# Kernel optimization log

Measured on AMD Instinct MI355X. Metric: run time of the kernel, lower is better.

## Reference

```python
import jax, jax.numpy as jnp
import numpy as np

# SparseSAKEEnergyModel: 6-layer sparse SAKE GNN (hidden=64, heads=4, update=False)
# followed by per-graph segment_sum and a Dense(64)->silu->Dense(1) head.
N_NODES = 10000
N_EDGES = 100000
F_IN = 16           # raw node feature dim (embedded to H by embedding_in)
H = 64              # hidden_features
HEADS = 4           # SAKE default n_heads
COEF = H * HEADS    # n_coefficients = 256
DEPTH = 6
RBF = 50            # ExpNormalSmearing num_rbf
CUT = 5.0           # ExpNormalSmearing cutoff_upper (alpha = 5/(5-0) = 1)
NUM_SEGMENTS = 100


def setup_inputs() -> dict:
    key = jax.random.key(0)
    ks = jax.random.split(key, 20)

    def dn(k, *shape):
        # Dense kernel init ~ lecun-normal-ish: std = 1/sqrt(fan_in); fan_in = shape[-2]
        return jax.random.normal(k, shape, jnp.float32) * np.float32(1.0 / np.sqrt(shape[-2]))

    start = float(np.exp(-CUT))
    rbf_means = jnp.broadcast_to(jnp.linspace(start, 1.0, RBF).astype(jnp.float32)[None], (DEPTH, RBF))
    rbf_betas = jnp.full((DEPTH, RBF), float(((2.0 / RBF) * (1.0 - start)) ** -2), jnp.float32)

    z = lambda *s: jnp.zeros(s, jnp.float32)
    return dict(
        i=jax.random.normal(ks[0], (N_NODES, F_IN), jnp.float32),
        x=jax.random.normal(ks[1], (N_NODES, 3), jnp.float32),
        emb_in_w=dn(ks[2], F_IN, H), emb_in_b=z(H),
        edge_in_w=dn(ks[3], DEPTH, 2 * H, RBF), edge_in_b=z(DEPTH, RBF),
        rbf_means=rbf_means, rbf_betas=rbf_betas,
        edge_out_w1=dn(ks[4], DEPTH, 2 * H + RBF + 1, H), edge_out_b1=z(DEPTH, H),
        edge_out_w2=dn(ks[5], DEPTH, H, H), edge_out_b2=z(DEPTH, H),
        sem_w=dn(ks[6], DEPTH, H, HEADS), sem_b=z(DEPTH, HEADS),
        xmix_w=dn(ks[7], DEPTH, COEF, COEF),
        pn_w1=dn(ks[8], DEPTH, COEF, H), pn_b1=z(DEPTH, H),
        pn_w2=dn(ks[9], DEPTH, H, H), pn_b2=z(DEPTH, H),
        node_w1=dn(ks[10], DEPTH, H + COEF + H, H), node_b1=z(DEPTH, H),
        node_w2=dn(ks[11], DEPTH, H, H), node_b2=z(DEPTH, H),
        emb_out_w1=dn(ks[12], H, H), emb_out_b1=z(H),
        emb_out_w2=dn(ks[13], H, H), emb_out_b2=z(H),
        head_w1=dn(ks[14], H, H), head_b1=z(H),
        head_w2=dn(ks[15], H, 1), head_b2=z(1),
        edges=jax.random.randint(ks[16], (N_EDGES, 2), 0, N_NODES, jnp.int32),
        graph_segments=jnp.sort(jax.random.randint(ks[17], (N_NODES,), 0, NUM_SEGMENTS, jnp.int32)),
    )


def _segment_softmax(logits, seg, num_segments):
    m = jax.ops.segment_max(logits, seg, num_segments)
    e = jnp.exp(logits - m[seg])
    s = jax.ops.segment_sum(e, seg, num_segments)
    return e / s[seg]


def _forward(i, x, emb_in_w, emb_in_b, edge_in_w, edge_in_b, rbf_means, rbf_betas,
             edge_out_w1, edge_out_b1, edge_out_w2, edge_out_b2, sem_w, sem_b, xmix_w,
             pn_w1, pn_b1, pn_w2, pn_b2, node_w1, node_b1, node_w2, node_b2,
             emb_out_w1, emb_out_b1, emb_out_w2, emb_out_b2,
             head_w1, head_b1, head_w2, head_b2, edges, graph_segments):
    N = x.shape[0]
    dst, src = edges[:, 0], edges[:, 1]
    x_minus_xt = x[dst] - x[src]                               # (E,3)
    d = jnp.sqrt((x_minus_xt ** 2).sum(-1, keepdims=True) + 1e-10)  # (E,1)
    dirs = x_minus_xt / (d + 1e-5)                             # normalized edge directions
    rbf_base = jnp.exp(-d)                                     # ExpNormalSmearing, alpha=1, lower=0

    h = i @ emb_in_w + emb_in_b                                # embedding_in -> (N,H)
    for l in range(DEPTH):
        # --- edge model: ContinuousFilterConvolutionWithConcatenation ---
        hc = jnp.concatenate([h[dst], h[src]], -1)             # (E,2H)
        hm = hc @ edge_in_w[l] + edge_in_b[l]                  # (E,RBF)
        rbf = jnp.exp(-rbf_betas[l] * (rbf_base - rbf_means[l]) ** 2)
        he = jnp.concatenate([hc, rbf * hm, d], -1)
        he = jax.nn.silu(he @ edge_out_w1[l] + edge_out_b1[l]) @ edge_out_w2[l] + edge_out_b2[l]  # (E,H)
        # --- combined (semantic * euclidean) attention, segment-softmax over dst ---
        att_s = _segment_softmax(jax.nn.celu(he @ sem_w[l] + sem_b[l], alpha=2.0), dst, N)  # (E,HEADS)
        att_e = _segment_softmax(-d, dst, N)                   # (E,1)
        att = att_e * att_s
        att = att / jax.ops.segment_sum(att, dst, N)[dst]
        hea = (he[:, :, None] * att[:, None, :]).reshape(-1, COEF)  # (E, H*HEADS)
        # --- spatial attention ---
        coef = jnp.tanh(hea @ xmix_w[l])                       # (E,COEF)
        csum = jax.ops.segment_sum(coef[:, :, None] * dirs[:, None, :], dst, N)  # (N,COEF,3)
        cnorm = (csum ** 2).sum(-1)                            # (N,COEF)
        h_comb = jax.nn.silu(jax.nn.silu(cnorm @ pn_w1[l] + pn_b1[l]) @ pn_w2[l] + pn_b2[l])
        # --- aggregate + node update (residual) ---
        h_agg = jax.ops.segment_sum(hea, dst, N)               # (N,COEF)
        upd = jnp.concatenate([h, h_agg, h_comb], -1)
        upd = jax.nn.silu(jax.nn.silu(upd @ node_w1[l] + node_b1[l]) @ node_w2[l] + node_b2[l])
        h = h + upd
    h = jax.nn.silu(h @ emb_out_w1 + emb_out_b1) @ emb_out_w2 + emb_out_b2  # embedding_out
    y = jax.ops.segment_sum(h, graph_segments, NUM_SEGMENTS)   # per-graph readout (G,H)
    return jax.nn.silu(y @ head_w1 + head_b1) @ head_w2 + head_b2  # (G,1)


def reference(i, x, emb_in_w, emb_in_b, edge_in_w, edge_in_b, rbf_means, rbf_betas,
              edge_out_w1, edge_out_b1, edge_out_w2, edge_out_b2, sem_w, sem_b, xmix_w,
              pn_w1, pn_b1, pn_w2, pn_b2, node_w1, node_b1, node_w2, node_b2,
              emb_out_w1, emb_out_b1, emb_out_w2, emb_out_b2,
              head_w1, head_b1, head_w2, head_b2, edges, graph_segments):
    return _forward(i, x, emb_in_w, emb_in_b, edge_in_w, edge_in_b, rbf_means, rbf_betas,
                    edge_out_w1, edge_out_b1, edge_out_w2, edge_out_b2, sem_w, sem_b, xmix_w,
                    pn_w1, pn_b1, pn_w2, pn_b2, node_w1, node_b1, node_w2, node_b2,
                    emb_out_w1, emb_out_b1, emb_out_w2, emb_out_b2,
                    head_w1, head_b1, head_w2, head_b2, edges, graph_segments)
```

## Files before the change

### kernel.cpp

```cpp
#include <hip/hip_runtime.h>
#include <hip/hip_bf16.h>

constexpr int EN   = 100000;
constexpr int NN   = 10000;
constexpr int DEPTH = 6;
constexpr int NSEG = 100;
constexpr int LP   = 40;

typedef unsigned short u16;
typedef __bf16 bf16x8 __attribute__((ext_vector_type(8)));
typedef float  f32x4  __attribute__((ext_vector_type(4)));

__device__ inline float wred_max(float v){
#pragma unroll
  for (int o = 32; o > 0; o >>= 1) v = fmaxf(v, __shfl_xor(v, o, 64));
  return v;
}
__device__ inline float wred_sum(float v){
#pragma unroll
  for (int o = 32; o > 0; o >>= 1) v += __shfl_xor(v, o, 64);
  return v;
}
__device__ inline float siluf(float x){ return x / (1.f + __expf(-x)); }
__device__ inline float fast_tanh(float x){
  float e = __expf(2.f * x);
  return 1.f - 2.f / (e + 1.f);
}
__device__ inline u16 f2bf(float x){
  unsigned u = __float_as_uint(x);
  u = u + 0x7FFFu + ((u >> 16) & 1u);
  return (u16)(u >> 16);
}
__device__ inline float bf2f(u16 u){
  union { float f; unsigned int ui; } v; v.ui = ((unsigned int)u) << 16; return v.f;
}
__device__ inline bf16x8 ldg_bf8(const u16* p){
  return *reinterpret_cast<const bf16x8*>(p);
}

__global__ __launch_bounds__(256) void count_k(const int* __restrict__ edges,
                                               int* __restrict__ counts){
  int e = blockIdx.x * 256 + threadIdx.x;
  if (e >= EN) return;
  atomicAdd(&counts[edges[2*e]], 1);
}

__global__ __launch_bounds__(256) void scan_k(const int* __restrict__ counts,
                                              int* __restrict__ offs){
  __shared__ int part[256];
  const int CH = (NN + 255) / 256;
  int t = threadIdx.x;
  int s = 0;
  for (int j = 0; j < CH; ++j){ int idx = t*CH + j; if (idx < NN) s += counts[idx]; }
  part[t] = s;
  __syncthreads();
  if (t == 0){
    int run = 0;
    for (int i = 0; i < 256; ++i){ int v = part[i]; part[i] = run; run += v; }
    offs[NN] = run;
  }
  __syncthreads();
  int run = part[t];
  for (int j = 0; j < CH; ++j){
    int idx = t*CH + j;
    if (idx < NN){ offs[idx] = run; run += counts[idx]; }
  }
}

__global__ __launch_bounds__(256) void geoscat_k(const int* __restrict__ edges,
                                                 const float* __restrict__ x,
                                                 const int* __restrict__ offs,
                                                 int* __restrict__ cursor,
                                                 int* __restrict__ edge_s,
                                                 float* __restrict__ dS,
                                                 float* __restrict__ dirsS,
                                                 float* __restrict__ rbfS){
  int e = blockIdx.x * 256 + threadIdx.x;
  if (e >= EN) return;
  int dst = edges[2*e], src = edges[2*e+1];
  float dx = x[dst*3+0] - x[src*3+0];
  float dy = x[dst*3+1] - x[src*3+1];
  float dz = x[dst*3+2] - x[src*3+2];
  float dd = sqrtf(dx*dx + dy*dy + dz*dz + 1e-10f);
  float inv = 1.f / (dd + 1e-5f);
  int pos = offs[dst] + atomicAdd(&cursor[dst], 1);
  edge_s[2*pos]   = dst;
  edge_s[2*pos+1] = src;
  dS[pos]   = dd;
  rbfS[pos] = __expf(-dd);
  dirsS[3*pos+0] = dx*inv; dirsS[3*pos+1] = dy*inv; dirsS[3*pos+2] = dz*inv;
}

__global__ __launch_bounds__(256) void h2b_k(const float* __restrict__ h,
                                             u16* __restrict__ hbf,
                                             u16* __restrict__ node_in){
  int gid = blockIdx.x * 256 + threadIdx.x;
  if (gid >= NN*64) return;
  int n = gid >> 6, ch = gid & 63;
  u16 b = f2bf(h[gid]);
  hbf[gid] = b;
  node_in[(size_t)n*384 + ch] = b;
}

__global__ void convw_k(const float* __restrict__ src, int K, int N, size_t sStride,
                        u16* __restrict__ dst, int Kpad, int Npad, size_t dStride){
  int idx = blockIdx.x * 256 + threadIdx.x;
  if (idx >= Npad*Kpad) return;
  int n = idx / Kpad, k = idx - n*Kpad;
  float v = (k < K && n < N) ? src[blockIdx.y*sStride + (size_t)k*N + n] : 0.f;
  dst[blockIdx.y*dStride + idx] = f2bf(v);
}

__global__ __launch_bounds__(256) void convx_k(const float* __restrict__ xmix,
                                               u16* __restrict__ xr){
  int idx = blockIdx.x * 256 + threadIdx.x;
  int l = blockIdx.y;
  int q  = idx & 63;
  int n  = (idx >> 6) & 255;
  int hd = idx >> 14;
  xr[(size_t)l*65536 + idx] = f2bf(xmix[(size_t)l*65536 + (size_t)(4*q + hd)*256 + n]);
}

__global__ __launch_bounds__(256) void edge_fused_k(
    const int* __restrict__ edge_s,
    const u16* __restrict__ hbf,
    const float* __restrict__ rbfS,
    const float* __restrict__ dS,
    const u16* __restrict__ Winb,
    const float* __restrict__ bin,
    const float* __restrict__ mean,
    const float* __restrict__ beta,
    const u16* __restrict__ W1b,
    const float* __restrict__ b1,
    const u16* __restrict__ W2b,
    const float* __restrict__ b2,
    const float* __restrict__ sw,
    const float* __restrict__ sb,
    u16* __restrict__ he,
    float* __restrict__ logit){
  __shared__ u16 HC[64*132];
  __shared__ u16 T2[64*72];
  __shared__ u16 HE1[64*72];
  const int tid = threadIdx.x, lane = tid & 63, wv = tid >> 6;
  const int l15 = lane & 15, kq = (lane >> 4) * 8;
  const int rsub = (lane >> 4) << 2;
  const int e0 = blockIdx.x * 64;
  const int nw = wv*16 + l15;

#pragma unroll
  for (int i = 0; i < 4; ++i){
    int idx = tid + i*256;
    int row = idx >> 4, c = idx & 15;
    int e = min(e0 + row, EN - 1);
    int node = (c < 8) ? edge_s[2*e] : edge_s[2*e+1];
    *reinterpret_cast<uint4*>(HC + row*132 + c*8) =
        *reinterpret_cast<const uint4*>(hbf + (size_t)node*64 + (c & 7)*8);
  }
  __syncthreads();

  f32x4 acc[4];
#pragma unroll
  for (int mt = 0; mt < 4; ++mt) acc[mt] = (f32x4){0.f,0.f,0.f,0.f};
#pragma unroll
  for (int kc = 0; kc < 128; kc += 32){
    bf16x8 bf = ldg_bf8(Winb + nw*128 + kc + kq);
#pragma unroll
    for (int mt = 0; mt < 4; ++mt){
      bf16x8 af = *reinterpret_cast<const bf16x8*>(HC + (mt*16 + l15)*132 + kc + kq);
      acc[mt] = __builtin_amdgcn_mfma_f32_16x16x32_bf16(af, bf, acc[mt], 0, 0, 0);
    }
  }
  {
    float bi = 0.f, mn = 0.f, bt = 0.f;
    if (nw < 50){ bi = bin[nw]; mn = mean[nw]; bt = beta[nw]; }
#pragma unroll
    for (int mt = 0; mt < 4; ++mt){
#pragma unroll
      for (int r = 0; r < 4; ++r){
        int row = mt*16 + rsub + r;
        int e = min(e0 + row, EN - 1);
        float v;
        if (nw < 50){ float df = rbfS[e] - mn; v = __expf(-bt*df*df) * (acc[mt][r] + bi); }
        else if (nw == 50) v = dS[e];
        else v = 0.f;
        T2[row*72 + nw] = f2bf(v);
      }
    }
  }
  __syncthreads();

#pragma unroll
  for (int mt = 0; mt < 4; ++mt) acc[mt] = (f32x4){0.f,0.f,0.f,0.f};
#pragma unroll
  for (int kc = 0; kc < 128; kc += 32){
    bf16x8 bf = ldg_bf8(W1b + nw*192 + kc + kq);
#pragma unroll
    for (int mt = 0; mt < 4; ++mt){
      bf16x8 af = *reinterpret_cast<const bf16x8*>(HC + (mt*16 + l15)*132 + kc + kq);
      acc[mt] = __builtin_amdgcn_mfma_f32_16x16x32_bf16(af, bf, acc[mt], 0, 0, 0);
    }
  }
#pragma unroll
  for (int kc = 128; kc < 192; kc += 32){
    bf16x8 bf = ldg_bf8(W1b + nw*192 + kc + kq);
#pragma unroll
    for (int mt = 0; mt < 4; ++mt){
      bf16x8 af = *reinterpret_cast<const bf16x8*>(T2 + (mt*16 + l15)*72 + (kc-128) + kq);
      acc[mt] = __builtin_amdgcn_mfma_f32_16x16x32_bf16(af, bf, acc[mt], 0, 0, 0);
    }
  }
  {
    float bb = b1[nw];
#pragma unroll
    for (int mt = 0; mt < 4; ++mt){
#pragma unroll
      for (int r = 0; r < 4; ++r){
        int row = mt*16 + rsub + r;
        HE1[row*72 + nw] = f2bf(siluf(acc[mt][r] + bb));
      }
    }
  }
  __syncthreads();

#pragma unroll
  for (int mt = 0; mt < 4; ++mt) acc[mt] = (f32x4){0.f,0.f,0.f,0.f};
#pragma unroll
  for (int kc = 0; kc < 64; kc += 32){
    bf16x8 bf = ldg_bf8(W2b + nw*64 + kc + kq);
#pragma unroll
    for (int mt = 0; mt < 4; ++mt){
      bf16x8 af = *reinterpret_cast<const bf16x8*>(HE1 + (mt*16 + l15)*72 + kc + kq);
      acc[mt] = __builtin_amdgcn_mfma_f32_16x16x32_bf16(af, bf, acc[mt], 0, 0, 0);
    }
  }
  {
    float bb = b2[nw];
#pragma unroll
    for (int mt = 0; mt < 4; ++mt){
#pragma unroll
      for (int r = 0; r < 4; ++r){
        int row = mt*16 + rsub + r;
        int e = e0 + row;
        u16 hb = f2bf(acc[mt][r] + bb);
        if (e < EN) he[(size_t)e*64 + nw] = hb;
        T2[row*72 + nw] = hb;
      }
    }
  }
  __syncthreads();

  {
    int er = tid >> 2, hd = tid & 3;
    float a = sb[hd];
#pragma unroll 8
    for (int k = 0; k < 64; ++k)
      a = fmaf(bf2f(T2[er*72 + k]), sw[k*4 + hd], a);
    float v = a > 0.f ? a : 2.f*(__expf(0.5f*a) - 1.f);
    int e = e0 + er;
    if (e < EN) logit[(size_t)e*4 + hd] = v;
  }
}

__global__ __launch_bounds__(256) void xmix_k(const u16* __restrict__ he,
                                              const float* __restrict__ att,
                                              const u16* __restrict__ Xr,
                                              u16* __restrict__ coef){
  __shared__ u16 B_s[2][128*72];
  const int tid = threadIdx.x, lane = tid & 63, wave = tid >> 6;
  const int l15 = lane & 15, kq = (lane >> 4) * 8;
  const int rsub = (lane >> 4) << 2;
  const int m0 = blockIdx.x * 128;
  const int n0 = blockIdx.y * 128;

  const int srow = tid >> 1;
  const int scol = (tid & 1) * 32;
  const u16* xsrc = Xr + ((size_t)(n0 + srow))*64 + scol;

  uint4 pf0 = *reinterpret_cast<const uint4*>(xsrc);
  uint4 pf1 = *reinterpret_cast<const uint4*>(xsrc + 8);
  uint4 pf2 = *reinterpret_cast<const uint4*>(xsrc + 16);
  uint4 pf3 = *reinterpret_cast<const uint4*>(xsrc + 24);

  float a32[2][2][8];
  float4 attA[2];
#pragma unroll
  for (int h = 0; h < 2; ++h){
    int m = min(m0 + h*64 + wave*16 + l15, EN - 1);
    attA[h] = *reinterpret_cast<const float4*>(att + (size_t)m*4);
#pragma unroll
    for (int k2 = 0; k2 < 2; ++k2){
      ushort4 u0 = *reinterpret_cast<const ushort4*>(he + (size_t)m*64 + k2*32 + kq);
      ushort4 u1 = *reinterpret_cast<const ushort4*>(he + (size_t)m*64 + k2*32 + kq + 4);
      a32[h][k2][0] = bf2f(u0.x); a32[h][k2][1] = bf2f(u0.y);
      a32[h][k2][2] = bf2f(u0.z); a32[h][k2][3] = bf2f(u0.w);
      a32[h][k2][4] = bf2f(u1.x); a32[h][k2][5] = bf2f(u1.y);
      a32[h][k2][6] = bf2f(u1.z); a32[h][k2][7] = bf2f(u1.w);
    }
  }

  f32x4 acc[2][8];
#pragma unroll
  for (int h = 0; h < 2; ++h)
#pragma unroll
    for (int c = 0; c < 8; ++c) acc[h][c] = (f32x4){0.f,0.f,0.f,0.f};

  {
    u16* dst = &B_s[0][srow*72 + scol];
    *reinterpret_cast<uint4*>(dst)      = pf0;
    *reinterpret_cast<uint4*>(dst + 8)  = pf1;
    *reinterpret_cast<uint4*>(dst + 16) = pf2;
    *reinterpret_cast<uint4*>(dst + 24) = pf3;
  }
  __syncthreads();

#pragma unroll
  for (int hd = 0; hd < 4; ++hd){
    if (hd < 3){
      const u16* s = xsrc + (size_t)(hd + 1) * 256 * 64;
      pf0 = *reinterpret_cast<const uint4*>(s);
      pf1 = *reinterpret_cast<const uint4*>(s + 8);
      pf2 = *reinterpret_cast<const uint4*>(s + 16);
      pf3 = *reinterpret_cast<const uint4*>(s + 24);
    }
    bf16x8 afs[2][2];
#pragma unroll
    for (int h = 0; h < 2; ++h){
      float a = (hd==0) ? attA[h].x : (hd==1) ? attA[h].y
              : (hd==2) ? attA[h].z : attA[h].w;
#pragma unroll
      for (int k2 = 0; k2 < 2; ++k2){
        u16 o[8];
#pragma unroll
        for (int j = 0; j < 8; ++j) o[j] = f2bf(a32[h][k2][j] * a);
        afs[h][k2] = *reinterpret_cast<bf16x8*>(o);
      }
    }
    const u16* Bb = &B_s[hd & 1][0];
#pragma unroll
    for (int k2 = 0; k2 < 2; ++k2){
#pragma unroll
      for (int c = 0; c < 8; ++c){
        bf16x8 bf = *reinterpret_cast<const bf16x8*>(Bb + (c*16 + l15)*72 + k2*32 + kq);
        acc[0][c] = __builtin_amdgcn_mfma_f32_16x16x32_bf16(afs[0][k2], bf, acc[0][c], 0, 0, 0);
        acc[1][c] = __builtin_amdgcn_mfma_f32_16x16x32_bf16(afs[1][k2], bf, acc[1][c], 0, 0, 0);
      }
    }
    if (hd < 3){
      u16* dst = &B_s[(hd + 1) & 1][srow*72 + scol];
      *reinterpret_cast<uint4*>(dst)      = pf0;
      *reinterpret_cast<uint4*>(dst + 8)  = pf1;
      *reinterpret_cast<uint4*>(dst + 16) = pf2;
      *reinterpret_cast<uint4*>(dst + 24) = pf3;
      __syncthreads();
    }
  }

#pragma unroll
  for (int h = 0; h < 2; ++h){
    const int rbase = m0 + h*64 + wave*16 + rsub;
#pragma unroll
    for (int c = 0; c < 8; ++c){
      int n = n0 + c*16 + l15;
#pragma unroll
      for (int r = 0; r < 4; ++r){
        int m = rbase + r;
        if (m < EN) coef[(size_t)m*256 + n] = f2bf(acc[h][c][r]);
      }
    }
  }
}

__global__ __launch_bounds__(256) void nodeblock_k(
    const u16* __restrict__ cnorm,
    const u16* __restrict__ P1t, const float* __restrict__ pb1,
    const u16* __restrict__ P2t, const float* __restrict__ pb2,
    const u16* __restrict__ node_in,
    const u16* __restrict__ N1t, const float* __restrict__ nb1,
    const u16* __restrict__ N2t, const float* __restrict__ nb2,
    const float* __restrict__ hres,
    float* __restrict__ hout,
    u16* __restrict__ hbf,
    u16* __restrict__ node_io){
  __shared__ u16 A_s[128*LP];
  __shared__ u16 B_s[64*LP];
  __shared__ u16 T_s[128*72];
  __shared__ u16 W2_s[64*72];
  __shared__ u16 HCm[128*72];
  const int tid = threadIdx.x, lane = tid & 63, wave = tid >> 6;
  const int m0 = blockIdx.x * 128;
  const int l15 = lane & 15, kq = (lane >> 4)*8;
  const int rsub = (lane >> 4) << 2;
  const int srow = tid >> 1, skh = (tid & 1)*16;
  const int arow = min(m0 + srow, NN - 1);
  const u16* aptr1 = cnorm + (size_t)arow*256 + skh;
  const u16* aptr2 = node_in + (size_t)arow*384 + skh;
  const int brow = tid >> 2, bcol = (tid & 3)*8;

#pragma unroll
  for (int i = 0; i < 2; ++i){
    int idx = tid + i*256;
    int row = idx >> 3, cc = (idx & 7)*8;
    *reinterpret_cast<uint4*>(W2_s + row*72 + cc) =
        *reinterpret_cast<const uint4*>(P2t + row*64 + cc);
  }

  f32x4 acc0[4], acc1[4];
#pragma unroll
  for (int c = 0; c < 4; ++c){ acc0[c] = (f32x4){0,0,0,0}; acc1[c] = (f32x4){0,0,0,0}; }

  for (int kc = 0; kc < 256; kc += 32){
    *reinterpret_cast<uint4*>(A_s + srow*LP + skh)     = *reinterpret_cast<const uint4*>(aptr1 + kc);
    *reinterpret_cast<uint4*>(A_s + srow*LP + skh + 8) = *reinterpret_cast<const uint4*>(aptr1 + kc + 8);
    *reinterpret_cast<uint4*>(B_s + brow*LP + bcol) =
        *reinterpret_cast<const uint4*>(P1t + (size_t)brow*256 + kc + bcol);
    __syncthreads();
    bf16x8 af0 = *reinterpret_cast<const bf16x8*>(A_s + (wave*16 + l15)*LP + kq);
    bf16x8 af1 = *reinterpret_cast<const bf16x8*>(A_s + (64 + wave*16 + l15)*LP + kq);
#pragma unroll
    for (int c = 0; c < 4; ++c){
      bf16x8 bf = *reinterpret_cast<const bf16x8*>(B_s + (c*16 + l15)*LP + kq);
      acc0[c] = __builtin_amdgcn_mfma_f32_16x16x32_bf16(af0, bf, acc0[c], 0, 0, 0);
      acc1[c] = __builtin_amdgcn_mfma_f32_16x16x32_bf16(af1, bf, acc1[c], 0, 0, 0);
    }
    __syncthreads();
  }
#pragma unroll
  for (int h = 0; h < 2; ++h){
#pragma unroll
    for (int c = 0; c < 4; ++c){
      int n = c*16 + l15;
      float bb = pb1[n];
#pragma unroll
      for (int r = 0; r < 4; ++r){
        int rowloc = h*64 + wave*16 + rsub + r;
        float a = (h == 0) ? acc0[c][r] : acc1[c][r];
        T_s[rowloc*72 + n] = f2bf(siluf(a + bb));
      }
    }
  }
  __syncthreads();
#pragma unroll
  for (int c = 0; c < 4; ++c){ acc0[c] = (f32x4){0,0,0,0}; acc1[c] = (f32x4){0,0,0,0}; }
#pragma unroll
  for (int kc = 0; kc < 64; kc += 32){
    bf16x8 af0 = *reinterpret_cast<const bf16x8*>(T_s + (wave*16 + l15)*72 + kc + kq);
    bf16x8 af1 = *reinterpret_cast<const bf16x8*>(T_s + (64 + wave*16 + l15)*72 + kc + kq);
#pragma unroll
    for (int c = 0; c < 4; ++c){
      bf16x8 bf = *reinterpret_cast<const bf16x8*>(W2_s + (c*16 + l15)*72 + kc + kq);
      acc0[c] = __builtin_amdgcn_mfma_f32_16x16x32_bf16(af0, bf, acc0[c], 0, 0, 0);
      acc1[c] = __builtin_amdgcn_mfma_f32_16x16x32_bf16(af1, bf, acc1[c], 0, 0, 0);
    }
  }
#pragma unroll
  for (int h = 0; h < 2; ++h){
#pragma unroll
    for (int c = 0; c < 4; ++c){
      int n = c*16 + l15;
      float bb = pb2[n];
#pragma unroll
      for (int r = 0; r < 4; ++r){
        int rowloc = h*64 + wave*16 + rsub + r;
        float a = (h == 0) ? acc0[c][r] : acc1[c][r];
        HCm[rowloc*72 + n] = f2bf(siluf(a + bb));
      }
    }
  }
  __syncthreads();

#pragma unroll
  for (int c = 0; c < 4; ++c){ acc0[c] = (f32x4){0,0,0,0}; acc1[c] = (f32x4){0,0,0,0}; }
  for (int kc = 0; kc < 320; kc += 32){
    *reinterpret_cast<uint4*>(A_s + srow*LP + skh)     = *reinterpret_cast<const uint4*>(aptr2 + kc);
    *reinterpret_cast<uint4*>(A_s + srow*LP + skh + 8) = *reinterpret_cast<const uint4*>(aptr2 + kc + 8);
    *reinterpret_cast<uint4*>(B_s + brow*LP + bcol) =
        *reinterpret_cast<const uint4*>(N1t + (size_t)brow*384 + kc + bcol);
    __syncthreads();
    bf16x8 af0 = *reinterpret_cast<const bf16x8*>(A_s + (wave*16 + l15)*LP + kq);
    bf16x8 af1 = *reinterpret_cast<const bf16x8*>(A_s + (64 + wave*16 + l15)*LP + kq);
#pragma unroll
    for (int c = 0; c < 4; ++c){
      bf16x8 bf = *reinterpret_cast<const bf16x8*>(B_s + (c*16 + l15)*LP + kq);
      acc0[c] = __builtin_amdgcn_mfma_f32_16x16x32_bf16(af0, bf, acc0[c], 0, 0, 0);
      acc1[c] = __builtin_amdgcn_mfma_f32_16x16x32_bf16(af1, bf, acc1[c], 0, 0, 0);
    }
    __syncthreads();
  }
#pragma unroll
  for (int kc = 320; kc < 384; kc += 32){
    bf16x8 af0 = *reinterpret_cast<const bf16x8*>(HCm + (wave*16 + l15)*72 + (kc-320) + kq);
    bf16x8 af1 = *reinterpret_cast<const bf16x8*>(HCm + (64 + wave*16 + l15)*72 + (kc-320) + kq);
#pragma unroll
    for (int c = 0; c < 4; ++c){
      bf16x8 bf = ldg_bf8(N1t + (size_t)(c*16 + l15)*384 + kc + kq);
      acc0[c] = __builtin_amdgcn_mfma_f32_16x16x32_bf16(af0, bf, acc0[c], 0, 0, 0);
      acc1[c] = __builtin_amdgcn_mfma_f32_16x16x32_bf16(af1, bf, acc1[c], 0, 0, 0);
    }
  }
#pragma unroll
  for (int h = 0; h < 2; ++h){
#pragma unroll
    for (int c = 0; c < 4; ++c){
      int n = c*16 + l15;
      float bb = nb1[n];
#pragma unroll
      for (int r = 0; r < 4; ++r){
        int rowloc = h*64 + wave*16 + rsub + r;
        float a = (h == 0) ? acc0[c][r] : acc1[c][r];
        T_s[rowloc*72 + n] = f2bf(siluf(a + bb));
      }
    }
  }
#pragma unroll
  for (int i = 0; i < 2; ++i){
    int idx = tid + i*256;
    int row = idx >> 3, cc = (idx & 7)*8;
    *reinterpret_cast<uint4*>(W2_s + row*72 + cc) =
        *reinterpret_cast<const uint4*>(N2t + row*64 + cc);
  }
  __syncthreads();
#pragma unroll
  for (int c = 0; c < 4; ++c){ acc0[c] = (f32x4){0,0,0,0}; acc1[c] = (f32x4){0,0,0,0}; }
#pragma unroll
  for (int kc = 0; kc < 64; kc += 32){
    bf16x8 af0 = *reinterpret_cast<const bf16x8*>(T_s + (wave*16 + l15)*72 + kc + kq);
    bf16x8 af1 = *reinterpret_cast<const bf16x8*>(T_s + (64 + wave*16 + l15)*72 + kc + kq);
#pragma unroll
    for (int c = 0; c < 4; ++c){
      bf16x8 bf = *reinterpret_cast<const bf16x8*>(W2_s + (c*16 + l15)*72 + kc + kq);
      acc0[c] = __builtin_amdgcn_mfma_f32_16x16x32_bf16(af0, bf, acc0[c], 0, 0, 0);
      acc1[c] = __builtin_amdgcn_mfma_f32_16x16x32_bf16(af1, bf, acc1[c], 0, 0, 0);
    }
  }
#pragma unroll
  for (int h = 0; h < 2; ++h){
#pragma unroll
    for (int c = 0; c < 4; ++c){
      int n = c*16 + l15;
      float bb = nb2[n];
#pragma unroll
      for (int r = 0; r < 4; ++r){
        int m = m0 + h*64 + wave*16 + rsub + r;
        if (m >= NN) continue;
        float a = (h == 0) ? acc0[c][r] : acc1[c][r];
        float hn = hres[(size_t)m*64 + n] + siluf(a + bb);
        hout[(size_t)m*64 + n] = hn;
        u16 bbf = f2bf(hn);
        hbf[(size_t)m*64 + n] = bbf;
        node_io[(size_t)m*384 + n] = bbf;
      }
    }
  }
}

__global__ __launch_bounds__(256) void mlp2_head_k(const u16* __restrict__ A,
                                                   const u16* __restrict__ W1t,
                                                   const float* __restrict__ b1,
                                                   const u16* __restrict__ W2t,
                                                   const float* __restrict__ b2,
                                                   float* __restrict__ outf){
  __shared__ u16 A_s[128*LP];
  __shared__ u16 B_s[64*LP];
  __shared__ u16 T_s[128*72];
  __shared__ u16 W2_s[64*72];
  const int tid = threadIdx.x, lane = tid & 63, wave = tid >> 6;
  const int m0 = blockIdx.x * 128;
  const int l15 = lane & 15, kq = (lane >> 4)*8;
  const int rsub = (lane >> 4) << 2;
#pragma unroll
  for (int i = 0; i < 2; ++i){
    int idx = tid + i*256;
    int row = idx >> 3, cc = (idx & 7)*8;
    *reinterpret_cast<uint4*>(W2_s + row*72 + cc) =
        *reinterpret_cast<const uint4*>(W2t + row*64 + cc);
  }
  const int srow = tid >> 1, skh = (tid & 1)*16;
  const int arow = min(m0 + srow, NN - 1);
  const u16* aptr = A + (size_t)arow*64 + skh;

  f32x4 acc0[4], acc1[4];
#pragma unroll
  for (int c = 0; c < 4; ++c){ acc0[c] = (f32x4){0,0,0,0}; acc1[c] = (f32x4){0,0,0,0}; }
  const int brow = tid >> 2, bcol = (tid & 3)*8;
  for (int kc = 0; kc < 64; kc += 32){
    *reinterpret_cast<uint4*>(A_s + srow*LP + skh)     = *reinterpret_cast<const uint4*>(aptr + kc);
    *reinterpret_cast<uint4*>(A_s + srow*LP + skh + 8) = *reinterpret_cast<const uint4*>(aptr + kc + 8);
    *reinterpret_cast<uint4*>(B_s + brow*LP + bcol) =
        *reinterpret_cast<const uint4*>(W1t + (size_t)brow*64 + kc + bcol);
    __syncthreads();
    bf16x8 af0 = *reinterpret_cast<const bf16x8*>(A_s + (wave*16 + l15)*LP + kq);
    bf16x8 af1 = *reinterpret_cast<const bf16x8*>(A_s + (64 + wave*16 + l15)*LP + kq);
#pragma unroll
    for (int c = 0; c < 4; ++c){
      bf16x8 bf = *reinterpret_cast<const bf16x8*>(B_s + (c*16 + l15)*LP + kq);
      acc0[c] = __builtin_amdgcn_mfma_f32_16x16x32_bf16(af0, bf, acc0[c], 0, 0, 0);
      acc1[c] = __builtin_amdgcn_mfma_f32_16x16x32_bf16(af1, bf, acc1[c], 0, 0, 0);
    }
    __syncthreads();
  }
#pragma unroll
  for (int h = 0; h < 2; ++h){
#pragma unroll
    for (int c = 0; c < 4; ++c){
      int n = c*16 + l15;
      float bb = b1[n];
#pragma unroll
      for (int r = 0; r < 4; ++r){
        int rowloc = h*64 + wave*16 + rsub + r;
        float a = (h == 0) ? acc0[c][r] : acc1[c][r];
        T_s[rowloc*72 + n] = f2bf(siluf(a + bb));
      }
    }
  }
  __syncthreads();
#pragma unroll
  for (int c = 0; c < 4; ++c){ acc0[c] = (f32x4){0,0,0,0}; acc1[c] = (f32x4){0,0,0,0}; }
#pragma unroll
  for (int kc = 0; kc < 64; kc += 32){
    bf16x8 af0 = *reinterpret_cast<const bf16x8*>(T_s + (wave*16 + l15)*72 + kc + kq);
    bf16x8 af1 = *reinterpret_cast<const bf16x8*>(T_s + (64 + wave*16 + l15)*72 + kc + kq);
#pragma unroll
    for (int c = 0; c < 4; ++c){
      bf16x8 bf = *reinterpret_cast<const bf16x8*>(W2_s + (c*16 + l15)*72 + kc + kq);
      acc0[c] = __builtin_amdgcn_mfma_f32_16x16x32_bf16(af0, bf, acc0[c], 0, 0, 0);
      acc1[c] = __builtin_amdgcn_mfma_f32_16x16x32_bf16(af1, bf, acc1[c], 0, 0, 0);
    }
  }
#pragma unroll
  for (int h = 0; h < 2; ++h){
#pragma unroll
    for (int c = 0; c < 4; ++c){
      int n = c*16 + l15;
      float bb = b2[n];
#pragma unroll
      for (int r = 0; r < 4; ++r){
        int m = m0 + h*64 + wave*16 + rsub + r;
        if (m >= NN) continue;
        float a = (h == 0) ? acc0[c][r] : acc1[c][r];
        outf[(size_t)m*64 + n] = a + bb;
      }
    }
  }
}

template<int EPI>
__global__ __launch_bounds__(256) void gemm_k(const float* __restrict__ A, int lda,
                                              const float* __restrict__ W, int ldw,
                                              const float* __restrict__ bias,
                                              float* __restrict__ out, int ldo, int ocol,
                                              int M, int N, int K){
  __shared__ float w_s[128*64];
  const int tid  = threadIdx.x;
  const int nl   = tid & 63;
  const int rg   = tid >> 6;
  const int col0 = blockIdx.y * 64;
  const int m0   = blockIdx.x * 16 + rg * 4;
  float acc[4] = {0.f, 0.f, 0.f, 0.f};
  const float* ar[4];
#pragma unroll
  for (int r = 0; r < 4; ++r){
    int mr = min(m0 + r, M - 1);
    ar[r] = A + (size_t)mr * lda;
  }
  for (int kc = 0; kc < K; kc += 128){
    int kn = min(128, K - kc);
    for (int idx = tid; idx < 128*64; idx += 256){
      int kk = idx >> 6, nn = idx & 63;
      int gn = col0 + nn;
      w_s[idx] = (kk < kn && gn < N) ? W[(size_t)(kc+kk)*ldw + gn] : 0.f;
    }
    __syncthreads();
    for (int k = 0; k < kn; ++k){
      float wv = w_s[k*64 + nl];
#pragma unroll
      for (int r = 0; r < 4; ++r) acc[r] = fmaf(ar[r][kc + k], wv, acc[r]);
    }
    __syncthreads();
  }
  int n = col0 + nl;
  if (n >= N) return;
  float b = bias ? bias[n] : 0.f;
#pragma unroll
  for (int r = 0; r < 4; ++r){
    int m = m0 + r;
    if (m >= M) break;
    float a = acc[r] + b;
    out[(size_t)m*ldo + ocol + n] = (EPI == 1) ? siluf(a) : a;
  }
}

__global__ __launch_bounds__(256) void att_k(const int* __restrict__ offs,
                                             const float* __restrict__ dS,
                                             const float* __restrict__ logit,
                                             float* __restrict__ att){
  int lane = threadIdx.x & 63;
  int node = (blockIdx.x * 256 + threadIdx.x) >> 6;
  if (node >= NN) return;
  int s0 = offs[node];
  int cnt = offs[node+1] - s0;
  if (cnt <= 0) return;
  const float NEG = -1e30f;
  if (cnt <= 64){
    bool act = lane < cnt;
    int p = s0 + (act ? lane : 0);
    float dd = dS[p];
    float4 lg = *reinterpret_cast<const float4*>(logit + 4*(size_t)p);
    float me  = wred_max(act ? -dd  : NEG);
    float ms0 = wred_max(act ? lg.x : NEG);
    float ms1 = wred_max(act ? lg.y : NEG);
    float ms2 = wred_max(act ? lg.z : NEG);
    float ms3 = wred_max(act ? lg.w : NEG);
    float ee  = act ? __expf(-dd - me)  : 0.f;
    float v0  = act ? __expf(lg.x - ms0) : 0.f;
    float v1  = act ? __expf(lg.y - ms1) : 0.f;
    float v2  = act ? __expf(lg.z - ms2) : 0.f;
    float v3  = act ? __expf(lg.w - ms3) : 0.f;
    float ise = 1.f / wred_sum(ee);
    float is0 = 1.f / wred_sum(v0);
    float is1 = 1.f / wred_sum(v1);
    float is2 = 1.f / wred_sum(v2);
    float is3 = 1.f / wred_sum(v3);
    float ae = ee * ise;
    float a0 = ae * v0 * is0, a1 = ae * v1 * is1;
    float a2 = ae * v2 * is2, a3 = ae * v3 * is3;
    float iz0 = 1.f / wred_sum(a0), iz1 = 1.f / wred_sum(a1);
    float iz2 = 1.f / wred_sum(a2), iz3 = 1.f / wred_sum(a3);
    if (act){
      float4 o; o.x = a0*iz0; o.y = a1*iz1; o.z = a2*iz2; o.w = a3*iz3;
      *reinterpret_cast<float4*>(att + 4*(size_t)p) = o;
    }
    return;
  }
  float me = NEG, ms0 = NEG, ms1 = NEG, ms2 = NEG, ms3 = NEG;
  for (int j = lane; j < cnt; j += 64){
    int p = s0 + j;
    float dd = dS[p];
    me = fmaxf(me, -dd);
    float4 lg = *reinterpret_cast<const float4*>(logit + 4*(size_t)p);
    ms0 = fmaxf(ms0, lg.x); ms1 = fmaxf(ms1, lg.y);
    ms2 = fmaxf(ms2, lg.z); ms3 = fmaxf(ms3, lg.w);
  }
  me = wred_max(me); ms0 = wred_max(ms0); ms1 = wred_max(ms1);
  ms2 = wred_max(ms2); ms3 = wred_max(ms3);
  float se = 0.f, ss0 = 0.f, ss1 = 0.f, ss2 = 0.f, ss3 = 0.f;
  for (int j = lane; j < cnt; j += 64){
    int p = s0 + j;
    float dd = dS[p];
    float4 lg = *reinterpret_cast<const float4*>(logit + 4*(size_t)p);
    se  += __expf(-dd - me);
    ss0 += __expf(lg.x - ms0); ss1 += __expf(lg.y - ms1);
    ss2 += __expf(lg.z - ms2); ss3 += __expf(lg.w - ms3);
  }
  se = wred_sum(se); ss0 = wred_sum(ss0); ss1 = wred_sum(ss1);
  ss2 = wred_sum(ss2); ss3 = wred_sum(ss3);
  float ise = 1.f/se, is0 = 1.f/ss0, is1 = 1.f/ss1, is2 = 1.f/ss2, is3 = 1.f/ss3;
  float z0 = 0.f, z1 = 0.f, z2 = 0.f, z3 = 0.f;
  for (int j = lane; j < cnt; j += 64){
    int p = s0 + j;
    float dd = dS[p];
    float4 lg = *reinterpret_cast<const float4*>(logit + 4*(size_t)p);
    float ae = __expf(-dd - me) * ise;
    z0 += ae * __expf(lg.x - ms0) * is0;
    z1 += ae * __expf(lg.y - ms1) * is1;
    z2 += ae * __expf(lg.z - ms2) * is2;
    z3 += ae * __expf(lg.w - ms3) * is3;
  }
  z0 = wred_sum(z0); z1 = wred_sum(z1); z2 = wred_sum(z2); z3 = wred_sum(z3);
  float iz0 = 1.f/z0, iz1 = 1.f/z1, iz2 = 1.f/z2, iz3 = 1.f/z3;
  for (int j = lane; j < cnt; j += 64){
    int p = s0 + j;
    float dd = dS[p];
    float4 lg = *reinterpret_cast<const float4*>(logit + 4*(size_t)p);
    float ae = __expf(-dd - me) * ise;
    float4 o;
    o.x = ae * __expf(lg.x - ms0) * is0 * iz0;
    o.y = ae * __expf(lg.y - ms1) * is1 * iz1;
    o.z = ae * __expf(lg.z - ms2) * is2 * iz2;
    o.w = ae * __expf(lg.w - ms3) * is3 * iz3;
    *reinterpret_cast<float4*>(att + 4*(size_t)p) = o;
  }
}

__global__ __launch_bounds__(256) void agg_k(const int* __restrict__ offs,
                                             const u16* __restrict__ coef,
                                             const u16* __restrict__ he,
                                             const float* __restrict__ att,
                                             const float* __restrict__ dirsS,
                                             u16* __restrict__ cnorm,
                                             u16* __restrict__ node_in){
  int node = blockIdx.x;
  int c = threadIdx.x;
  int s0 = offs[node], s1 = offs[node+1];
  int q = c >> 2, hd = c & 3;
  float cs0 = 0.f, cs1 = 0.f, cs2 = 0.f, ha = 0.f;
  int p = s0;
  for (; p + 2 <= s1; p += 2){
    float co0 = fast_tanh(bf2f(coef[(size_t)p*256 + c]));
    float co1 = fast_tanh(bf2f(coef[(size_t)(p+1)*256 + c]));
    float hv0 = bf2f(he[(size_t)p*64 + q]);
    float hv1 = bf2f(he[(size_t)(p+1)*64 + q]);
    float av0 = att[(size_t)p*4 + hd];
    float av1 = att[(size_t)(p+1)*4 + hd];
    float d00 = dirsS[3*(size_t)p],     d01 = dirsS[3*(size_t)p+1],     d02 = dirsS[3*(size_t)p+2];
    float d10 = dirsS[3*(size_t)(p+1)], d11 = dirsS[3*(size_t)(p+1)+1], d12 = dirsS[3*(size_t)(p+1)+2];
    cs0 = fmaf(co0, d00, cs0); cs1 = fmaf(co0, d01, cs1); cs2 = fmaf(co0, d02, cs2);
    cs0 = fmaf(co1, d10, cs0); cs1 = fmaf(co1, d11, cs1); cs2 = fmaf(co1, d12, cs2);
    ha = fmaf(hv0, av0, ha);
    ha = fmaf(hv1, av1, ha);
  }
  if (p < s1){
    float co = fast_tanh(bf2f(coef[(size_t)p*256 + c]));
    float hv = bf2f(he[(size_t)p*64 + q]);
    float av = att[(size_t)p*4 + hd];
    float d0 = dirsS[3*(size_t)p], d1 = dirsS[3*(size_t)p+1], d2 = dirsS[3*(size_t)p+2];
    cs0 = fmaf(co, d0, cs0); cs1 = fmaf(co, d1, cs1); cs2 = fmaf(co, d2, cs2);
    ha = fmaf(hv, av, ha);
  }
  cnorm[(size_t)node*256 + c] = f2bf(cs0*cs0 + cs1*cs1 + cs2*cs2);
  node_in[(size_t)node*384 + 64 + c] = f2bf(ha);
}

__global__ __launch_bounds__(256) void segy_k(const float* __restrict__ hf,
                                              const int* __restrict__ seg,
                                              float* __restrict__ y){
  int gid = blockIdx.x * 256 + threadIdx.x;
  if (gid >= NN*64) return;
  int n = gid >> 6, ch = gid & 63;
  atomicAdd(&y[seg[n]*64 + ch], hf[gid]);
}

__global__ void headf_k(const float* __restrict__ t2,
                        const float* __restrict__ w2,
                        const float* __restrict__ b2,
                        float* __restrict__ out){
  int s = threadIdx.x;
  if (s >= NSEG) return;
  float acc = b2[0];
  for (int k = 0; k < 64; ++k) acc = fmaf(t2[s*64 + k], w2[k], acc);
  out[s] = acc;
}

extern "C" void kernel_launch(void* const* d_in, const int* in_sizes, int n_in,
                              void* d_out, int out_size, void* d_ws, size_t ws_size,
                              hipStream_t stream) {
  (void)in_sizes; (void)n_in; (void)out_size; (void)ws_size;
  const float* in_i       = (const float*)d_in[0];
  const float* in_x       = (const float*)d_in[1];
  const float* emb_in_w   = (const float*)d_in[2];
  const float* emb_in_b   = (const float*)d_in[3];
  const float* edge_in_w  = (const float*)d_in[4];
  const float* edge_in_b  = (const float*)d_in[5];
  const float* rbf_means  = (const float*)d_in[6];
  const float* rbf_betas  = (const float*)d_in[7];
  const float* edge_o_w1  = (const float*)d_in[8];
  const float* edge_o_b1  = (const float*)d_in[9];
  const float* edge_o_w2  = (const float*)d_in[10];
  const float* edge_o_b2  = (const float*)d_in[11];
  const float* sem_w      = (const float*)d_in[12];
  const float* sem_b      = (const float*)d_in[13];
  const float* xmix_w     = (const float*)d_in[14];
  const float* pn_w1      = (const float*)d_in[15];
  const float* pn_b1      = (const float*)d_in[16];
  const float* pn_w2      = (const float*)d_in[17];
  const float* pn_b2      = (const float*)d_in[18];
  const float* node_w1    = (const float*)d_in[19];
  const float* node_b1    = (const float*)d_in[20];
  const float* node_w2    = (const float*)d_in[21];
  const float* node_b2    = (const float*)d_in[22];
  const float* emb_o_w1   = (const float*)d_in[23];
  const float* emb_o_b1   = (const float*)d_in[24];
  const float* emb_o_w2   = (const float*)d_in[25];
  const float* emb_o_b2   = (const float*)d_in[26];
  const float* head_w1    = (const float*)d_in[27];
  const float* head_b1    = (const float*)d_in[28];
  const float* head_w2    = (const float*)d_in[29];
  const float* head_b2    = (const float*)d_in[30];
  const int*   edges      = (const int*)d_in[31];
  const int*   segs       = (const int*)d_in[32];
  float* out = (float*)d_out;

  char* base = (char*)d_ws;
  size_t off = 0;
  auto alloc = [&](size_t bytes) -> void* {
    void* p = base + off;
    off += (bytes + 255) & ~(size_t)255;
    return p;
  };
  float* dS     = (float*)alloc((size_t)EN*4);
  float* dirsS  = (float*)alloc((size_t)EN*3*4);
  float* rbfS   = (float*)alloc((size_t)EN*4);
  int*   edge_s = (int*)alloc((size_t)EN*2*4);
  float* hA     = (float*)alloc((size_t)NN*64*4);
  float* hB     = (float*)alloc((size_t)NN*64*4);
  u16*   he     = (u16*)alloc((size_t)EN*64*2);
  u16*   coef   = (u16*)alloc((size_t)EN*256*2);
  float* logit  = (float*)alloc((size_t)EN*4*4);
  float* att    = (float*)alloc((size_t)EN*4*4);
  u16*   hbf    = (u16*)alloc((size_t)NN*64*2);
  u16*   node_in= (u16*)alloc((size_t)NN*384*2);
  u16*   cnorm  = (u16*)alloc((size_t)NN*256*2);
  float* y      = (float*)alloc((size_t)NSEG*64*4);
  float* t2     = (float*)alloc((size_t)NSEG*64*4);
  u16* winb  = (u16*)alloc((size_t)DEPTH*64*128*2);
  u16* w1b   = (u16*)alloc((size_t)DEPTH*64*192*2);
  u16* w2b   = (u16*)alloc((size_t)DEPTH*64*64*2);
  u16* xr    = (u16*)alloc((size_t)DEPTH*4*256*64*2);
  u16* pw1b  = (u16*)alloc((size_t)DEPTH*64*256*2);
  u16* pw2b  = (u16*)alloc((size_t)DEPTH*64*64*2);
  u16* nw1b  = (u16*)alloc((size_t)DEPTH*64*384*2);
  u16* nw2b  = (u16*)alloc((size_t)DEPTH*64*64*2);
  u16* eo1b  = (u16*)alloc((size_t)64*64*2);
  u16* eo2b  = (u16*)alloc((size_t)64*64*2);
  int* counts   = (int*)alloc((size_t)NN*4);
  int* cursor   = (int*)alloc((size_t)NN*4);
  int* offs     = (int*)alloc((size_t)(NN+1)*4);

  hipMemsetAsync(counts, 0, (size_t)NN*4, stream);
  hipMemsetAsync(cursor, 0, (size_t)NN*4, stream);
  hipMemsetAsync(y, 0, (size_t)NSEG*64*4, stream);

  count_k<<<(EN+255)/256, 256, 0, stream>>>(edges, counts);
  scan_k<<<1, 256, 0, stream>>>(counts, offs);
  geoscat_k<<<(EN+255)/256, 256, 0, stream>>>(edges, in_x, offs, cursor,
                                              edge_s, dS, dirsS, rbfS);

  convw_k<<<dim3(32,  DEPTH), 256, 0, stream>>>(edge_in_w, 128, 50, (size_t)128*50, winb, 128, 64, (size_t)64*128);
  convw_k<<<dim3(48,  DEPTH), 256, 0, stream>>>(edge_o_w1, 179, 64, (size_t)179*64, w1b,  192, 64, (size_t)64*192);
  convw_k<<<dim3(16,  DEPTH), 256, 0, stream>>>(edge_o_w2,  64, 64, (size_t)64*64,  w2b,   64, 64, (size_t)64*64);
  convx_k<<<dim3(256, DEPTH), 256, 0, stream>>>(xmix_w, xr);
  convw_k<<<dim3(64,  DEPTH), 256, 0, stream>>>(pn_w1,     256, 64, (size_t)256*64, pw1b, 256, 64, (size_t)64*256);
  convw_k<<<dim3(16,  DEPTH), 256, 0, stream>>>(pn_w2,      64, 64, (size_t)64*64,  pw2b,  64, 64, (size_t)64*64);
  convw_k<<<dim3(96,  DEPTH), 256, 0, stream>>>(node_w1,   384, 64, (size_t)384*64, nw1b, 384, 64, (size_t)64*384);
  convw_k<<<dim3(16,  DEPTH), 256, 0, stream>>>(node_w2,    64, 64, (size_t)64*64,  nw2b,  64, 64, (size_t)64*64);
  convw_k<<<dim3(16,  1),     256, 0, stream>>>(emb_o_w1,   64, 64, (size_t)64*64,  eo1b,  64, 64, (size_t)64*64);
  convw_k<<<dim3(16,  1),     256, 0, stream>>>(emb_o_w2,   64, 64, (size_t)64*64,  eo2b,  64, 64, (size_t)64*64);

  gemm_k<0><<<dim3((NN+15)/16, 1), 256, 0, stream>>>(
      in_i, 16, emb_in_w, 64, emb_in_b, hA, 64, 0, NN, 64, 16);
  h2b_k<<<(NN*64)/256, 256, 0, stream>>>(hA, hbf, node_in);

  const int EB  = (EN + 63) / 64;
  const int EB2 = (EN + 127) / 128;
  const int NB2 = (NN + 127) / 128;

  float* hcur = hA;
  float* hnext = hB;
  for (int l = 0; l < DEPTH; ++l){
    const float* bin  = edge_in_b + (size_t)l*50;
    const float* mean = rbf_means + (size_t)l*50;
    const float* beta = rbf_betas + (size_t)l*50;
    const float* b1   = edge_o_b1 + (size_t)l*64;
    const float* b2   = edge_o_b2 + (size_t)l*64;
    const float* sw   = sem_w + (size_t)l*64*4;
    const float* sb   = sem_b + (size_t)l*4;
    const float* pb1  = pn_b1 + (size_t)l*64;
    const float* pb2  = pn_b2 + (size_t)l*64;
    const float* nb1  = node_b1 + (size_t)l*64;
    const float* nb2  = node_b2 + (size_t)l*64;
    const u16* Winb = winb + (size_t)l*64*128;
    const u16* W1b  = w1b  + (size_t)l*64*192;
    const u16* W2b  = w2b  + (size_t)l*64*64;
    const u16* Xrl  = xr   + (size_t)l*65536;
    const u16* P1b  = pw1b + (size_t)l*64*256;
    const u16* P2b  = pw2b + (size_t)l*64*64;
    const u16* N1b  = nw1b + (size_t)l*64*384;
    const u16* N2b  = nw2b + (size_t)l*64*64;

    edge_fused_k<<<EB, 256, 0, stream>>>(edge_s, hbf, rbfS, dS,
                                         Winb, bin, mean, beta,
                                         W1b, b1, W2b, b2, sw, sb,
                                         he, logit);
    att_k<<<(NN+3)/4, 256, 0, stream>>>(offs, dS, logit, att);
    xmix_k<<<dim3(EB2, 2), 256, 0, stream>>>(he, att, Xrl, coef);
    agg_k<<<NN, 256, 0, stream>>>(offs, coef, he, att, dirsS, cnorm, node_in);
    nodeblock_k<<<NB2, 256, 0, stream>>>(cnorm, P1b, pb1, P2b, pb2,
                                         node_in, N1b, nb1, N2b, nb2,
                                         hcur, hnext, hbf, node_in);
    float* tmp = hcur; hcur = hnext; hnext = tmp;
  }

  mlp2_head_k<<<NB2, 256, 0, stream>>>(hbf, eo1b, emb_o_b1, eo2b, emb_o_b2, hnext);
  segy_k<<<(NN*64)/256, 256, 0, stream>>>(hnext, segs, y);
  gemm_k<1><<<dim3((NSEG+15)/16, 1), 256, 0, stream>>>(
      y, 64, head_w1, 64, head_b1, t2, 64, 0, NSEG, 64, 64);
  headf_k<<<1, 128, 0, stream>>>(t2, head_w2, head_b2, out);
}
```

Before: 931.4 us.

## Retile xmix kernel so each wave owns a 64-column slice with private LDS

```diff
diff --git a/kernel.cpp b/kernel.cpp
--- a/kernel.cpp
+++ b/kernel.cpp
@@ -265,106 +265,77 @@
                                               const float* __restrict__ att,
                                               const u16* __restrict__ Xr,
                                               u16* __restrict__ coef){
-  __shared__ u16 B_s[2][128*72];
+  __shared__ u16 B_s[4][64*72];
   const int tid = threadIdx.x, lane = tid & 63, wave = tid >> 6;
   const int l15 = lane & 15, kq = (lane >> 4) * 8;
   const int rsub = (lane >> 4) << 2;
-  const int m0 = blockIdx.x * 128;
-  const int n0 = blockIdx.y * 128;
-
-  const int srow = tid >> 1;
-  const int scol = (tid & 1) * 32;
-  const u16* xsrc = Xr + ((size_t)(n0 + srow))*64 + scol;
-
-  uint4 pf0 = *reinterpret_cast<const uint4*>(xsrc);
-  uint4 pf1 = *reinterpret_cast<const uint4*>(xsrc + 8);
-  uint4 pf2 = *reinterpret_cast<const uint4*>(xsrc + 16);
-  uint4 pf3 = *reinterpret_cast<const uint4*>(xsrc + 24);
-
-  float a32[2][2][8];
-  float4 attA[2];
-#pragma unroll
-  for (int h = 0; h < 2; ++h){
-    int m = min(m0 + h*64 + wave*16 + l15, EN - 1);
-    attA[h] = *reinterpret_cast<const float4*>(att + (size_t)m*4);
+  const int m0 = blockIdx.x * 64;
+  const int n0 = wave * 64;
+
+  bf16x8 araw[4][2];
+  float4 attA[4];
+#pragma unroll
+  for (int s = 0; s < 4; ++s){
+    int m = min(m0 + s*16 + l15, EN - 1);
+    attA[s] = *reinterpret_cast<const float4*>(att + (size_t)m*4);
+#pragma unroll
+    for (int k2 = 0; k2 < 2; ++k2)
+      araw[s][k2] = *reinterpret_cast<const bf16x8*>(he + (size_t)m*64 + k2*32 + kq);
+  }
+
+  f32x4 acc[4][4];
+#pragma unroll
+  for (int s = 0; s < 4; ++s)
+#pragma unroll
+    for (int c = 0; c < 4; ++c) acc[s][c] = (f32x4){0.f,0.f,0.f,0.f};
+
+  u16* Bw = &B_s[wave][0];
+
+#pragma unroll
+  for (int hd = 0; hd < 4; ++hd){
+    {
+      const u16* src = Xr + ((size_t)hd*256 + n0 + lane)*64;
+      u16* dst = Bw + lane*72;
+#pragma unroll
+      for (int j = 0; j < 8; ++j)
+        *reinterpret_cast<uint4*>(dst + j*8) = *reinterpret_cast<const uint4*>(src + j*8);
+    }
+    bf16x8 afs[4][2];
+#pragma unroll
+    for (int s = 0; s < 4; ++s){
+      float a = (hd==0) ? attA[s].x : (hd==1) ? attA[s].y
+              : (hd==2) ? attA[s].z : attA[s].w;
+#pragma unroll
+      for (int k2 = 0; k2 < 2; ++k2){
+        const u16* rp = reinterpret_cast<const u16*>(&araw[s][k2]);
+        u16 o[8];
+#pragma unroll
+        for (int j = 0; j < 8; ++j) o[j] = f2bf(bf2f(rp[j]) * a);
+        afs[s][k2] = *reinterpret_cast<bf16x8*>(o);
+      }
+    }
 #pragma unroll
     for (int k2 = 0; k2 < 2; ++k2){
-      ushort4 u0 = *reinterpret_cast<const ushort4*>(he + (size_t)m*64 + k2*32 + kq);
-      ushort4 u1 = *reinterpret_cast<const ushort4*>(he + (size_t)m*64 + k2*32 + kq + 4);
-      a32[h][k2][0] = bf2f(u0.x); a32[h][k2][1] = bf2f(u0.y);
-      a32[h][k2][2] = bf2f(u0.z); a32[h][k2][3] = bf2f(u0.w);
-      a32[h][k2][4] = bf2f(u1.x); a32[h][k2][5] = bf2f(u1.y);
-      a32[h][k2][6] = bf2f(u1.z); a32[h][k2][7] = bf2f(u1.w);
-    }
-  }
-
-  f32x4 acc[2][8];
-#pragma unroll
-  for (int h = 0; h < 2; ++h)
-#pragma unroll
-    for (int c = 0; c < 8; ++c) acc[h][c] = (f32x4){0.f,0.f,0.f,0.f};
-
-  {
-    u16* dst = &B_s[0][srow*72 + scol];
-    *reinterpret_cast<uint4*>(dst)      = pf0;
-    *reinterpret_cast<uint4*>(dst + 8)  = pf1;
-    *reinterpret_cast<uint4*>(dst + 16) = pf2;
-    *reinterpret_cast<uint4*>(dst + 24) = pf3;
-  }
-  __syncthreads();
-
-#pragma unroll
-  for (int hd = 0; hd < 4; ++hd){
-    if (hd < 3){
-      const u16* s = xsrc + (size_t)(hd + 1) * 256 * 64;
-      pf0 = *reinterpret_cast<const uint4*>(s);
-      pf1 = *reinterpret_cast<const uint4*>(s + 8);
-      pf2 = *reinterpret_cast<const uint4*>(s + 16);
-      pf3 = *reinterpret_cast<const uint4*>(s + 24);
-    }
-    bf16x8 afs[2][2];
-#pragma unroll
-    for (int h = 0; h < 2; ++h){
-      float a = (hd==0) ? attA[h].x : (hd==1) ? attA[h].y
-              : (hd==2) ? attA[h].z : attA[h].w;
-#pragma unroll
-      for (int k2 = 0; k2 < 2; ++k2){
-        u16 o[8];
-#pragma unroll
-        for (int j = 0; j < 8; ++j) o[j] = f2bf(a32[h][k2][j] * a);
-        afs[h][k2] = *reinterpret_cast<bf16x8*>(o);
-      }
-    }
-    const u16* Bb = &B_s[hd & 1][0];
-#pragma unroll
-    for (int k2 = 0; k2 < 2; ++k2){
-#pragma unroll
-      for (int c = 0; c < 8; ++c){
-        bf16x8 bf = *reinterpret_cast<const bf16x8*>(Bb + (c*16 + l15)*72 + k2*32 + kq);
-        acc[0][c] = __builtin_amdgcn_mfma_f32_16x16x32_bf16(afs[0][k2], bf, acc[0][c], 0, 0, 0);
-        acc[1][c] = __builtin_amdgcn_mfma_f32_16x16x32_bf16(afs[1][k2], bf, acc[1][c], 0, 0, 0);
-      }
-    }
-    if (hd < 3){
-      u16* dst = &B_s[(hd + 1) & 1][srow*72 + scol];
-      *reinterpret_cast<uint4*>(dst)      = pf0;
-      *reinterpret_cast<uint4*>(dst + 8)  = pf1;
-      *reinterpret_cast<uint4*>(dst + 16) = pf2;
-      *reinterpret_cast<uint4*>(dst + 24) = pf3;
-      __syncthreads();
-    }
-  }
-
-#pragma unroll
-  for (int h = 0; h < 2; ++h){
-    const int rbase = m0 + h*64 + wave*16 + rsub;
-#pragma unroll
-    for (int c = 0; c < 8; ++c){
+#pragma unroll
+      for (int c = 0; c < 4; ++c){
+        bf16x8 bf = *reinterpret_cast<const bf16x8*>(Bw + (c*16 + l15)*72 + k2*32 + kq);
+#pragma unroll
+        for (int s = 0; s < 4; ++s)
+          acc[s][c] = __builtin_amdgcn_mfma_f32_16x16x32_bf16(afs[s][k2], bf, acc[s][c], 0, 0, 0);
+      }
+    }
+  }
+
+#pragma unroll
+  for (int s = 0; s < 4; ++s){
+    const int rbase = m0 + s*16 + rsub;
+#pragma unroll
+    for (int c = 0; c < 4; ++c){
       int n = n0 + c*16 + l15;
 #pragma unroll
       for (int r = 0; r < 4; ++r){
         int m = rbase + r;
-        if (m < EN) coef[(size_t)m*256 + n] = f2bf(acc[h][c][r]);
+        if (m < EN) coef[(size_t)m*256 + n] = f2bf(acc[s][c][r]);
       }
     }
   }
@@ -940,7 +911,6 @@
   h2b_k<<<(NN*64)/256, 256, 0, stream>>>(hA, hbf, node_in);
 
   const int EB  = (EN + 63) / 64;
-  const int EB2 = (EN + 127) / 128;
   const int NB2 = (NN + 127) / 128;
 
   float* hcur = hA;
@@ -971,7 +941,7 @@
                                          W1b, b1, W2b, b2, sw, sb,
                                          he, logit);
     att_k<<<(NN+3)/4, 256, 0, stream>>>(offs, dS, logit, att);
-    xmix_k<<<dim3(EB2, 2), 256, 0, stream>>>(he, att, Xrl, coef);
+    xmix_k<<<EB, 256, 0, stream>>>(he, att, Xrl, coef);
     agg_k<<<NN, 256, 0, stream>>>(offs, coef, he, att, dirsS, cnorm, node_in);
     nodeblock_k<<<NB2, 256, 0, stream>>>(cnorm, P1b, pb1, P2b, pb2,
                                          node_in, N1b, nb1, N2b, nb2,
```

New measurement: 1.014 ms. +8.8%, slower.
